# Optimization experiments

Hardware: AMD Instinct MI355X
Metric: run time of the kernel (lower is better)

The kernel has to match this reference:

```python
import jax, jax.numpy as jnp
import numpy as np

B, N, D = 16, 2048, 4        # batch, input points, input feature dim (x,y,e1,e2)
G = 45                        # folding grid side -> M = G*G = 2025 output points
M = G * G
CW = 512                      # codeword dim
H1, H2 = 64, 128              # encoder hidden dims
FH = 512                      # folding MLP hidden dim


def _glorot(key, shape):
    fan_in, fan_out = shape[0], shape[1]
    s = jnp.sqrt(2.0 / (fan_in + fan_out)).astype(jnp.float32)
    return jax.random.normal(key, shape, dtype=jnp.float32) * s


def setup_inputs() -> dict:
    key = jax.random.key(0)
    ks = jax.random.split(key, 16)
    inp = {
        "points": jax.random.normal(ks[0], (B, N, D), dtype=jnp.float32),
        # encoder shared MLP: D -> H1 -> H2 -> CW, max-pool over N
        "ew1": _glorot(ks[1], (D, H1)),  "eb1": jnp.zeros((H1,), jnp.float32),
        "ew2": _glorot(ks[2], (H1, H2)), "eb2": jnp.zeros((H2,), jnp.float32),
        "ew3": _glorot(ks[3], (H2, CW)), "eb3": jnp.zeros((CW,), jnp.float32),
        # folding decoder
        "f1w1": _glorot(ks[4], (CW + 2, FH)), "f1b1": jnp.zeros((FH,), jnp.float32),
        "f1w2": _glorot(ks[5], (FH, FH)),     "f1b2": jnp.zeros((FH,), jnp.float32),
        "f1w3": _glorot(ks[6], (FH, 3)),      "f1b3": jnp.zeros((3,), jnp.float32),
        "f2w1": _glorot(ks[7], (CW + 3, FH)), "f2b1": jnp.zeros((FH,), jnp.float32),
        "f2w2": _glorot(ks[8], (FH, FH)),     "f2b2": jnp.zeros((FH,), jnp.float32),
        "f2w3": _glorot(ks[9], (FH, 3)),      "f2b3": jnp.zeros((3,), jnp.float32),
    }
    # fixed 2D folding grid in [-0.3, 0.3]^2, (M, 2)
    lin = jnp.linspace(-0.3, 0.3, G, dtype=jnp.float32)
    gx, gy = jnp.meshgrid(lin, lin, indexing="ij")
    inp["grid"] = jnp.stack([gx.ravel(), gy.ravel()], axis=-1)
    return inp


def _encode(points, ew1, eb1, ew2, eb2, ew3, eb3):
    h = jax.nn.relu(points @ ew1 + eb1)     # (B, N, H1)
    h = jax.nn.relu(h @ ew2 + eb2)          # (B, N, H2)
    h = h @ ew3 + eb3                       # (B, N, CW)
    return jnp.max(h, axis=1)               # (B, CW) codeword theta


def _decode(theta, grid, f1w1, f1b1, f1w2, f1b2, f1w3, f1b3,
            f2w1, f2b1, f2w2, f2b2, f2w3, f2b3):
    th = jnp.broadcast_to(theta[:, None, :], (theta.shape[0], M, CW))
    g = jnp.broadcast_to(grid[None], (theta.shape[0], M, 2))
    # folding 1: (codeword, 2D grid) -> 3D
    x = jnp.concatenate([th, g], axis=-1)
    x = jax.nn.relu(x @ f1w1 + f1b1)
    x = jax.nn.relu(x @ f1w2 + f1b2)
    fold1 = x @ f1w3 + f1b3                 # (B, M, 3)
    # folding 2: (codeword, intermediate 3D) -> 3D
    x = jnp.concatenate([th, fold1], axis=-1)
    x = jax.nn.relu(x @ f2w1 + f2b1)
    x = jax.nn.relu(x @ f2w2 + f2b2)
    return x @ f2w3 + f2b3                  # (B, M, 3)


def _chamfer(a, b):
    # a: (B, N, 3), b: (B, M, 3); squared-distance chamfer, both directions
    a2 = jnp.sum(a * a, axis=-1)                          # (B, N)
    b2 = jnp.sum(b * b, axis=-1)                          # (B, M)
    ab = jnp.einsum("bnd,bmd->bnm", a, b)                  # (B, N, M)
    d2 = a2[:, :, None] + b2[:, None, :] - 2.0 * ab
    d2 = jnp.maximum(d2, 0.0)
    return jnp.mean(jnp.min(d2, axis=2)) + jnp.mean(jnp.min(d2, axis=1))


def reference(points, ew1, eb1, ew2, eb2, ew3, eb3, grid,
              f1w1, f1b1, f1w2, f1b2, f1w3, f1b3,
              f2w1, f2b1, f2w2, f2b2, f2w3, f2b3):
    theta = _encode(points, ew1, eb1, ew2, eb2, ew3, eb3)
    pc_out = _decode(theta, grid, f1w1, f1b1, f1w2, f1b2, f1w3, f1b3,
                     f2w1, f2b1, f2w2, f2b2, f2w3, f2b3)
    # pc_input: (x, y, sum of energy channels)  -> (B, N, 3)
    energy = jnp.sum(points[:, :, 2:], axis=-1, keepdims=True)
    pc_input = jnp.concatenate([points[:, :, :2], energy], axis=-1)
    loss = _chamfer(pc_input, pc_out)
    return theta, pc_out, loss
```

## Files before the change

### kernel.cpp

```cpp
#include <hip/hip_runtime.h>

#define NBATCH 16
#define NPTS   2048
#define MQ     2025
#define CWDIM  512
#define NROWS  32400

typedef __attribute__((ext_vector_type(8))) short bf16x8;
typedef __attribute__((ext_vector_type(4))) float f32x4;

__device__ __forceinline__ unsigned fkey(float f) {
  unsigned u = __float_as_uint(f);
  return (u & 0x80000000u) ? ~u : (u | 0x80000000u);
}
__device__ __forceinline__ float funkey(unsigned u) {
  unsigned v = (u & 0x80000000u) ? (u ^ 0x80000000u) : ~u;
  return __uint_as_float(v);
}
__device__ __forceinline__ unsigned short f2bf(float f) {
  unsigned u = __float_as_uint(f);
  u = (u + 0x7FFFu + ((u >> 16) & 1u)) >> 16;
  return (unsigned short)u;
}

__global__ __launch_bounds__(256) void prep_kernel(
    const float* __restrict__ ew2, const float* __restrict__ ew3,
    const float* __restrict__ f1w2, const float* __restrict__ f2w2,
    unsigned short* __restrict__ ew2T, unsigned short* __restrict__ ew3C,
    unsigned short* __restrict__ w2C, unsigned* __restrict__ zws)
{
  __shared__ float tile[32][33];
  const int blk = blockIdx.x;
  const int t = threadIdx.x;

  if (blk < 8) {
    const int kt = blk >> 2, nt = blk & 3;
    const int tx = t & 31, ty = t >> 5;
    #pragma unroll
    for (int j = 0; j < 4; ++j)
      tile[ty + 8 * j][tx] = ew2[(size_t)(kt * 32 + ty + 8 * j) * 128 + nt * 32 + tx];
    __syncthreads();
    #pragma unroll
    for (int j = 0; j < 4; ++j)
      ew2T[(size_t)(nt * 32 + ty + 8 * j) * 64 + kt * 32 + tx] = f2bf(tile[tx][ty + 8 * j]);
  } else if (blk < 40) {
    const int gid = (blk - 8) * 256 + t;
    const int c16 = gid & 15, hi = (gid >> 4) & 3, cblk = (gid >> 6) & 31, kblk = gid >> 11;
    const int col = cblk * 16 + c16;
    unsigned short tmp[8];
    #pragma unroll
    for (int j = 0; j < 8; ++j)
      tmp[j] = f2bf(ew3[(size_t)(kblk * 32 + hi * 8 + j) * 512 + col]);
    int4 pk;
    pk.x = (int)((unsigned)tmp[0] | ((unsigned)tmp[1] << 16));
    pk.y = (int)((unsigned)tmp[2] | ((unsigned)tmp[3] << 16));
    pk.z = (int)((unsigned)tmp[4] | ((unsigned)tmp[5] << 16));
    pk.w = (int)((unsigned)tmp[6] | ((unsigned)tmp[7] << 16));
    *(int4*)&ew3C[(size_t)gid * 8] = pk;
  } else if (blk < 296) {
    const int gid = (blk - 40) * 256 + t;
    const int s = gid >> 15;
    const int rem = gid & 32767;
    const int c16 = rem & 15, hi = (rem >> 4) & 3, cblk = (rem >> 6) & 31, kt = rem >> 11;
    const int col = cblk * 16 + c16;
    const float* src = s ? f2w2 : f1w2;
    unsigned short tmp[8];
    #pragma unroll
    for (int j = 0; j < 8; ++j)
      tmp[j] = f2bf(src[(size_t)(kt * 32 + hi * 8 + j) * 512 + col]);
    int4 pk;
    pk.x = (int)((unsigned)tmp[0] | ((unsigned)tmp[1] << 16));
    pk.y = (int)((unsigned)tmp[2] | ((unsigned)tmp[3] << 16));
    pk.z = (int)((unsigned)tmp[4] | ((unsigned)tmp[5] << 16));
    pk.w = (int)((unsigned)tmp[6] | ((unsigned)tmp[7] << 16));
    *(int4*)&w2C[(size_t)s * 262144 + (size_t)rem * 8] = pk;
  } else {
    const int idx = (blk - 296) * 256 + t;
    for (int i = idx; i < 24640; i += 6144) zws[i] = 0u;
  }
}

__global__ __launch_bounds__(512, 2) void enc2_kernel(
    const float* __restrict__ pts,
    const float* __restrict__ ew1, const float* __restrict__ eb1,
    const unsigned short* __restrict__ ew2T, const float* __restrict__ eb2,
    const unsigned short* __restrict__ ew3C, const float* __restrict__ eb3,
    unsigned* __restrict__ keys)
{
  __shared__ unsigned short h1s[64 * 64];
  __shared__ unsigned short h2s[64 * 128];
  __shared__ float s_pts[64][4];
  const int t = threadIdx.x;
  const int b = blockIdx.x >> 5, p0 = (blockIdx.x & 31) << 6;
  if (t < 64)
    *(float4*)&s_pts[t][0] = *(const float4*)(pts + ((size_t)b * NPTS + p0 + t) * 4);
  __syncthreads();

  {
    const int c = t & 63;
    const float w0 = ew1[c], w1 = ew1[64 + c], w2 = ew1[128 + c], w3 = ew1[192 + c];
    const float bb = eb1[c];
    #pragma unroll
    for (int i = 0; i < 8; ++i) {
      const int p = i * 8 + (t >> 6);
      float acc = bb + s_pts[p][0] * w0 + s_pts[p][1] * w1 + s_pts[p][2] * w2 + s_pts[p][3] * w3;
      unsigned byte = ((unsigned)p << 7) + ((unsigned)c << 1);
      byte ^= ((unsigned)(p & 7)) << 4;
      h1s[byte >> 1] = f2bf(fmaxf(acc, 0.f));
    }
  }
  __syncthreads();

  const int wv = t >> 6, lane = t & 63, l15 = lane & 15, hi = lane >> 4;

  {
    f32x4 acc[4];
    #pragma unroll
    for (int m = 0; m < 4; ++m) acc[m] = (f32x4){0.f, 0.f, 0.f, 0.f};
    const int col = 16 * wv + l15;
    #pragma unroll
    for (int kk = 0; kk < 64; kk += 32) {
      bf16x8 bv = *(const bf16x8*)(ew2T + (size_t)col * 64 + kk + hi * 8);
      #pragma unroll
      for (int m = 0; m < 4; ++m) {
        const int row = 16 * m + l15;
        unsigned byte = ((unsigned)row << 7) + ((unsigned)((kk + hi * 8)) << 1);
        byte ^= ((unsigned)(row & 7)) << 4;
        bf16x8 av = *(const bf16x8*)&h1s[byte >> 1];
        acc[m] = __builtin_amdgcn_mfma_f32_16x16x32_bf16(av, bv, acc[m], 0, 0, 0);
      }
    }
    const float b2c = eb2[col];
    #pragma unroll
    for (int m = 0; m < 4; ++m)
      #pragma unroll
      for (int r = 0; r < 4; ++r) {
        const int row = 16 * m + hi * 4 + r;
        unsigned byte = ((unsigned)row << 8) + ((unsigned)col << 1);
        byte ^= ((unsigned)(row & 7)) << 4;
        h2s[byte >> 1] = f2bf(fmaxf(acc[m][r] + b2c, 0.f));
      }
  }
  __syncthreads();

  {
    f32x4 acc[4][4];
    #pragma unroll
    for (int m = 0; m < 4; ++m)
      #pragma unroll
      for (int n = 0; n < 4; ++n) acc[m][n] = (f32x4){0.f, 0.f, 0.f, 0.f};
    #pragma unroll
    for (int kk = 0; kk < 128; kk += 32) {
      bf16x8 av[4];
      #pragma unroll
      for (int m = 0; m < 4; ++m) {
        const int row = 16 * m + l15;
        unsigned byte = ((unsigned)row << 8) + ((unsigned)(kk + hi * 8) << 1);
        byte ^= ((unsigned)(row & 7)) << 4;
        av[m] = *(const bf16x8*)&h2s[byte >> 1];
      }
      #pragma unroll
      for (int n = 0; n < 4; ++n) {
        bf16x8 bv = *(const bf16x8*)(ew3C +
            (size_t)(((kk >> 5) * 32 + 4 * wv + n) * 512) + lane * 8);
        #pragma unroll
        for (int m = 0; m < 4; ++m)
          acc[m][n] = __builtin_amdgcn_mfma_f32_16x16x32_bf16(av[m], bv, acc[m][n], 0, 0, 0);
      }
    }
    #pragma unroll
    for (int n = 0; n < 4; ++n) {
      const int col = 64 * wv + 16 * n + l15;
      float mx = -1e30f;
      #pragma unroll
      for (int m = 0; m < 4; ++m)
        #pragma unroll
        for (int r = 0; r < 4; ++r) mx = fmaxf(mx, acc[m][n][r]);
      mx = fmaxf(mx, __shfl_xor(mx, 16));
      mx = fmaxf(mx, __shfl_xor(mx, 32));
      if (hi == 0) atomicMax(&keys[b * CWDIM + col], fkey(mx + eb3[col]));
    }
  }
}

__global__ __launch_bounds__(256) void h1base_kernel(
    const unsigned* __restrict__ keys, float* __restrict__ theta_out,
    const float* __restrict__ f1w1, const float* __restrict__ f1b1,
    const float* __restrict__ f2w1, const float* __restrict__ f2b1,
    float* __restrict__ h1b)
{
  __shared__ float thl[256];
  const int t = threadIdx.x;
  const int gid = blockIdx.x * 256 + t;
  const int half = gid >> 14;
  const int rem = gid & 16383;
  const int stage = rem >> 13, bb = (rem >> 9) & 15, c = rem & 511;
  thl[t] = funkey(keys[bb * 512 + half * 256 + t]);
  if (gid < 8192) theta_out[gid] = funkey(keys[gid]);
  __syncthreads();
  const float* w = stage ? f2w1 : f1w1;
  float acc = (half == 0) ? (stage ? f2b1[c] : f1b1[c]) : 0.f;
  const float* wp = w + (size_t)(half * 256) * 512 + c;
  #pragma unroll 8
  for (int k = 0; k < 256; ++k) acc += thl[k] * wp[(size_t)k * 512];
  atomicAdd(&h1b[rem], acc);
}

struct Fold5Smem {
  unsigned short sA[64 * 512];
  float red[8][32][3];
  float ext[64][4];
  int   rowbb[64];
};

template <int ST>
__device__ __forceinline__ void fold5_stage(Fold5Smem& S, int t, int r0,
    const float* __restrict__ h1bg,
    const float* __restrict__ w1,
    const unsigned short* __restrict__ wst,
    const float* __restrict__ b2, const float* __restrict__ w3,
    const float* __restrict__ b3, float* __restrict__ out_pc)
{
  constexpr int NE = ST ? 3 : 2;
  const int wv = t >> 6, lane = t & 63, l15 = lane & 15, hi = lane >> 4;
  const int wm = wv >> 2, wn = wv & 3;

  __syncthreads();

  {
    const int row = t & 63;
    const int bb = S.rowbb[row];
    const float e0 = S.ext[row][0], e1 = S.ext[row][1];
    float e2 = 0.f;
    if (NE == 3) e2 = S.ext[row][2];
    const float* hb  = h1bg + ST * 8192 + bb * 512;
    const float* wr0 = w1 + (size_t)512 * 512;
    const float* wr1 = wr0 + 512;
    const float* wr2 = wr1 + 512;
    #pragma unroll
    for (int i = 0; i < 8; ++i) {
      const int ko = (t >> 6) * 8 + i;
      const int c0 = ko * 8;
      float v[8];
      #pragma unroll
      for (int hf = 0; hf < 2; ++hf) {
        float4 h = *(const float4*)(hb + c0 + hf * 4);
        float4 a = *(const float4*)(wr0 + c0 + hf * 4);
        float4 bq = *(const float4*)(wr1 + c0 + hf * 4);
        v[hf * 4 + 0] = h.x + e0 * a.x + e1 * bq.x;
        v[hf * 4 + 1] = h.y + e0 * a.y + e1 * bq.y;
        v[hf * 4 + 2] = h.z + e0 * a.z + e1 * bq.z;
        v[hf * 4 + 3] = h.w + e0 * a.w + e1 * bq.w;
        if (NE == 3) {
          float4 cq = *(const float4*)(wr2 + c0 + hf * 4);
          v[hf * 4 + 0] += e2 * cq.x; v[hf * 4 + 1] += e2 * cq.y;
          v[hf * 4 + 2] += e2 * cq.z; v[hf * 4 + 3] += e2 * cq.w;
        }
      }
      int4 pk;
      pk.x = (int)((unsigned)f2bf(fmaxf(v[0], 0.f)) | ((unsigned)f2bf(fmaxf(v[1], 0.f)) << 16));
      pk.y = (int)((unsigned)f2bf(fmaxf(v[2], 0.f)) | ((unsigned)f2bf(fmaxf(v[3], 0.f)) << 16));
      pk.z = (int)((unsigned)f2bf(fmaxf(v[4], 0.f)) | ((unsigned)f2bf(fmaxf(v[5], 0.f)) << 16));
      pk.w = (int)((unsigned)f2bf(fmaxf(v[6], 0.f)) | ((unsigned)f2bf(fmaxf(v[7], 0.f)) << 16));
      *(int4*)&S.sA[(unsigned)(((ko >> 2) * 4 + (row >> 4)) * 512 + (ko & 3) * 128 + (row & 15) * 8)] = pk;
    }
  }
  __syncthreads();

  float p[2][4][3];
  #pragma unroll
  for (int m = 0; m < 2; ++m)
    #pragma unroll
    for (int r = 0; r < 4; ++r)
      #pragma unroll
      for (int jj = 0; jj < 3; ++jj) p[m][r][jj] = 0.f;

  #pragma unroll 1
  for (int pass = 0; pass < 2; ++pass) {
    f32x4 acc[2][4];
    #pragma unroll
    for (int m = 0; m < 2; ++m)
      #pragma unroll
      for (int n = 0; n < 4; ++n) acc[m][n] = (f32x4){0.f, 0.f, 0.f, 0.f};

    const unsigned short* wb = wst + (size_t)(pass * 16 + wn * 4) * 512 + lane * 8;

    #pragma unroll 2
    for (int kt = 0; kt < 16; ++kt) {
      bf16x8 bv[4];
      #pragma unroll
      for (int n = 0; n < 4; ++n)
        bv[n] = *(const bf16x8*)(wb + (size_t)(kt * 32 + n) * 512);
      const unsigned abase = (unsigned)(kt * 4 + 2 * wm) * 512 + (unsigned)lane * 8;
      bf16x8 a0 = *(const bf16x8*)&S.sA[abase];
      bf16x8 a1 = *(const bf16x8*)&S.sA[abase + 512];
      __builtin_amdgcn_s_setprio(1);
      #pragma unroll
      for (int n = 0; n < 4; ++n) {
        acc[0][n] = __builtin_amdgcn_mfma_f32_16x16x32_bf16(a0, bv[n], acc[0][n], 0, 0, 0);
        acc[1][n] = __builtin_amdgcn_mfma_f32_16x16x32_bf16(a1, bv[n], acc[1][n], 0, 0, 0);
      }
      __builtin_amdgcn_s_setprio(0);
    }

    #pragma unroll
    for (int n = 0; n < 4; ++n) {
      const int colG = pass * 256 + wn * 64 + 16 * n + l15;
      const float b2c = b2[colG];
      const float w30 = w3[colG * 3 + 0], w31 = w3[colG * 3 + 1], w32 = w3[colG * 3 + 2];
      #pragma unroll
      for (int m = 0; m < 2; ++m)
        #pragma unroll
        for (int r = 0; r < 4; ++r) {
          const float h = fmaxf(acc[m][n][r] + b2c, 0.f);
          p[m][r][0] += h * w30; p[m][r][1] += h * w31; p[m][r][2] += h * w32;
        }
    }
  }

  #pragma unroll
  for (int m = 0; m < 2; ++m)
    #pragma unroll
    for (int r = 0; r < 4; ++r)
      #pragma unroll
      for (int jj = 0; jj < 3; ++jj) {
        float v = p[m][r][jj];
        v += __shfl_xor(v, 1); v += __shfl_xor(v, 2);
        v += __shfl_xor(v, 4); v += __shfl_xor(v, 8);
        p[m][r][jj] = v;
      }
  if (l15 == 0) {
    #pragma unroll
    for (int m = 0; m < 2; ++m)
      #pragma unroll
      for (int r = 0; r < 4; ++r) {
        const int rl = 16 * m + hi * 4 + r;
        S.red[wv][rl][0] = p[m][r][0];
        S.red[wv][rl][1] = p[m][r][1];
        S.red[wv][rl][2] = p[m][r][2];
      }
  }
  __syncthreads();

  if (t < 192) {
    const int row = t / 3, jj = t - (t / 3) * 3;
    const int wg = (row >> 5) * 4, rl = row & 31;
    float v = b3[jj] + S.red[wg][rl][jj] + S.red[wg + 1][rl][jj]
                     + S.red[wg + 2][rl][jj] + S.red[wg + 3][rl][jj];
    if (ST == 0) S.ext[row][jj] = v;
    else if (r0 + row < NROWS) out_pc[(size_t)(r0 + row) * 3 + jj] = v;
  }
  __syncthreads();
}

__global__ __launch_bounds__(512, 2) void fold5_kernel(
    const float* __restrict__ grid2, const float* __restrict__ h1b,
    const unsigned short* __restrict__ w2C,
    const float* __restrict__ f1w1, const float* __restrict__ f1b2,
    const float* __restrict__ f1w3, const float* __restrict__ f1b3,
    const float* __restrict__ f2w1, const float* __restrict__ f2b2,
    const float* __restrict__ f2w3, const float* __restrict__ f2b3,
    float* __restrict__ out_pc)
{
  __shared__ Fold5Smem S;
  const int t = threadIdx.x;
  const int r0 = blockIdx.x * 64;

  if (t < 64) {
    const int r = r0 + t;
    const int bb = min(r / MQ, NBATCH - 1);
    S.rowbb[t] = bb;
    const int m = min(r - bb * MQ, MQ - 1);
    S.ext[t][0] = grid2[m * 2 + 0];
    S.ext[t][1] = grid2[m * 2 + 1];
    S.ext[t][2] = 0.f;
    S.ext[t][3] = 0.f;
  }

  fold5_stage<0>(S, t, r0, h1b, f1w1, w2C,          f1b2, f1w3, f1b3, nullptr);
  fold5_stage<1>(S, t, r0, h1b, f2w1, w2C + 262144, f2b2, f2w3, f2b3, out_pc);
}

__global__ __launch_bounds__(256) void cham_kernel(
    const float* __restrict__ pts, const float* __restrict__ pc,
    float* __restrict__ lacc, float* __restrict__ loss)
{
  __shared__ float s0[2048], s1[2048], s2[2048];
  const int t = threadIdx.x;
  const int side = blockIdx.x >> 9;
  const int ib = blockIdx.x & 511;
  const int b = ib >> 5;

  if (side == 0) {
    const int n0 = (ib & 31) << 6;
    const float* pcb = pc + (size_t)b * (MQ * 3);
    for (int i = t; i < MQ * 3; i += 256) {
      float v = pcb[i];
      int m = i / 3, j = i - m * 3;
      if (j == 0) s0[m] = v; else if (j == 1) s1[m] = v; else s2[m] = v;
    }
    for (int i = MQ + t; i < 2048; i += 256) { s0[i] = 1e30f; s1[i] = 1e30f; s2[i] = 1e30f; }
    __syncthreads();

    const int pid = t >> 4, q = t & 15;
    float ax[4], ay[4], az[4], mn[4];
    #pragma unroll
    for (int j = 0; j < 4; ++j) {
      const int n = n0 + pid * 4 + j;
      float4 P = *(const float4*)(pts + ((size_t)b * NPTS + n) * 4);
      ax[j] = P.x; ay[j] = P.y; az[j] = P.z + P.w; mn[j] = 1e30f;
    }
    #pragma unroll 4
    for (int i = 0; i < 32; ++i) {
      const int m4 = q * 4 + i * 64;
      float4 bx = *(const float4*)&s0[m4];
      float4 by = *(const float4*)&s1[m4];
      float4 bz = *(const float4*)&s2[m4];
      #pragma unroll
      for (int j = 0; j < 4; ++j) {
        float d0, dx, dy, dz;
        dx = ax[j] - bx.x; dy = ay[j] - by.x; dz = az[j] - bz.x; d0 = dx*dx + dy*dy + dz*dz; mn[j] = fminf(mn[j], d0);
        dx = ax[j] - bx.y; dy = ay[j] - by.y; dz = az[j] - bz.y; d0 = dx*dx + dy*dy + dz*dz; mn[j] = fminf(mn[j], d0);
        dx = ax[j] - bx.z; dy = ay[j] - by.z; dz = az[j] - bz.z; d0 = dx*dx + dy*dy + dz*dz; mn[j] = fminf(mn[j], d0);
        dx = ax[j] - bx.w; dy = ay[j] - by.w; dz = az[j] - bz.w; d0 = dx*dx + dy*dy + dz*dz; mn[j] = fminf(mn[j], d0);
      }
    }
    #pragma unroll
    for (int j = 0; j < 4; ++j) {
      mn[j] = fminf(mn[j], __shfl_xor(mn[j], 1));
      mn[j] = fminf(mn[j], __shfl_xor(mn[j], 2));
      mn[j] = fminf(mn[j], __shfl_xor(mn[j], 4));
      mn[j] = fminf(mn[j], __shfl_xor(mn[j], 8));
    }
    float v = (q == 0) ? (mn[0] + mn[1] + mn[2] + mn[3]) : 0.f;
    v += __shfl_xor(v, 16); v += __shfl_xor(v, 32);
    if ((t & 63) == 0) atomicAdd(lacc, v);
  } else {
    const int m0 = (ib & 31) << 6;
    for (int i = t; i < NPTS; i += 256) {
      float4 pp = *(const float4*)(pts + ((size_t)b * NPTS + i) * 4);
      s0[i] = pp.x; s1[i] = pp.y; s2[i] = pp.z + pp.w;
    }
    __syncthreads();

    const int pid = t >> 4, q = t & 15;
    float bx[4], by[4], bz[4], mn[4];
    bool vld[4];
    #pragma unroll
    for (int j = 0; j < 4; ++j) {
      const int m = m0 + pid * 4 + j;
      vld[j] = (m < MQ);
      const int mc = vld[j] ? m : (MQ - 1);
      bx[j] = pc[(size_t)b * (MQ * 3) + mc * 3 + 0];
      by[j] = pc[(size_t)b * (MQ * 3) + mc * 3 + 1];
      bz[j] = pc[(size_t)b * (MQ * 3) + mc * 3 + 2];
      mn[j] = 1e30f;
    }
    #pragma unroll 4
    for (int i = 0; i < 32; ++i) {
      const int n4 = q * 4 + i * 64;
      float4 axv = *(const float4*)&s0[n4];
      float4 ayv = *(const float4*)&s1[n4];
      float4 azv = *(const float4*)&s2[n4];
      #pragma unroll
      for (int j = 0; j < 4; ++j) {
        float d0, dx, dy, dz;
        dx = axv.x - bx[j]; dy = ayv.x - by[j]; dz = azv.x - bz[j]; d0 = dx*dx + dy*dy + dz*dz; mn[j] = fminf(mn[j], d0);
        dx = axv.y - bx[j]; dy = ayv.y - by[j]; dz = azv.y - bz[j]; d0 = dx*dx + dy*dy + dz*dz; mn[j] = fminf(mn[j], d0);
        dx = axv.z - bx[j]; dy = ayv.z - by[j]; dz = azv.z - bz[j]; d0 = dx*dx + dy*dy + dz*dz; mn[j] = fminf(mn[j], d0);
        dx = axv.w - bx[j]; dy = ayv.w - by[j]; dz = azv.w - bz[j]; d0 = dx*dx + dy*dy + dz*dz; mn[j] = fminf(mn[j], d0);
      }
    }
    #pragma unroll
    for (int j = 0; j < 4; ++j) {
      mn[j] = fminf(mn[j], __shfl_xor(mn[j], 1));
      mn[j] = fminf(mn[j], __shfl_xor(mn[j], 2));
      mn[j] = fminf(mn[j], __shfl_xor(mn[j], 4));
      mn[j] = fminf(mn[j], __shfl_xor(mn[j], 8));
    }
    float v = 0.f;
    if (q == 0) {
      #pragma unroll
      for (int j = 0; j < 4; ++j) if (vld[j]) v += mn[j];
    }
    v += __shfl_xor(v, 16); v += __shfl_xor(v, 32);
    if ((t & 63) == 0) atomicAdd(lacc + 1, v);
  }

  __syncthreads();
  if (t == 0) {
    __threadfence();
    unsigned old = atomicAdd((unsigned*)(lacc + 2), 1u);
    if (old == 1023u) {
      float l0 = atomicAdd(lacc, 0.f);
      float l1 = atomicAdd(lacc + 1, 0.f);
      loss[0] = l0 * (1.0f / (NBATCH * NPTS)) + l1 * (1.0f / (NBATCH * MQ));
    }
  }
}

extern "C" void kernel_launch(void* const* d_in, const int* in_sizes, int n_in,
                              void* d_out, int out_size, void* d_ws, size_t ws_size,
                              hipStream_t stream) {
  const float* pts  = (const float*)d_in[0];
  const float* ew1  = (const float*)d_in[1];
  const float* eb1  = (const float*)d_in[2];
  const float* ew2  = (const float*)d_in[3];
  const float* eb2  = (const float*)d_in[4];
  const float* ew3  = (const float*)d_in[5];
  const float* eb3  = (const float*)d_in[6];
  const float* f1w1 = (const float*)d_in[7];
  const float* f1b1 = (const float*)d_in[8];
  const float* f1w2 = (const float*)d_in[9];
  const float* f1b2 = (const float*)d_in[10];
  const float* f1w3 = (const float*)d_in[11];
  const float* f1b3 = (const float*)d_in[12];
  const float* f2w1 = (const float*)d_in[13];
  const float* f2b1 = (const float*)d_in[14];
  const float* f2w2 = (const float*)d_in[15];
  const float* f2b2 = (const float*)d_in[16];
  const float* f2w3 = (const float*)d_in[17];
  const float* f2b3 = (const float*)d_in[18];
  const float* grid2= (const float*)d_in[19];

  float* out = (float*)d_out;
  unsigned* keys       = (unsigned*)d_ws;
  float* lacc          = (float*)((char*)d_ws + 32768);
  float* h1b           = (float*)((char*)d_ws + 33024);
  unsigned short* w2C  = (unsigned short*)((char*)d_ws + 98560);
  unsigned short* ew2T = (unsigned short*)((char*)d_ws + 1147136);
  unsigned short* ew3C = (unsigned short*)((char*)d_ws + 1163520);

  prep_kernel<<<320, 256, 0, stream>>>(ew2, ew3, f1w2, f2w2,
                                       ew2T, ew3C, w2C, (unsigned*)d_ws);
  enc2_kernel<<<512, 512, 0, stream>>>(pts, ew1, eb1, ew2T, eb2, ew3C, eb3, keys);
  h1base_kernel<<<128, 256, 0, stream>>>(keys, out, f1w1, f1b1, f2w1, f2b1, h1b);
  fold5_kernel<<<507, 512, 0, stream>>>(grid2, h1b, w2C,
                                        f1w1, f1b2, f1w3, f1b3,
                                        f2w1, f2b2, f2w3, f2b3,
                                        out + 8192);
  cham_kernel<<<1024, 256, 0, stream>>>(pts, out + 8192, lacc,
                                        out + 8192 + 97200);
}
```

Before: 253.4 us.

## Widen fold MFMA tiles per wave and use expanded-norm chamfer distances

The fold kernel now has each of the 8 waves compute all 64 rows against its own 64 output columns in a single pass. This replaces the 2x4 wave split that needed two passes, so each wave loads each weight tile once and reuses it across four A tiles. The cost is 64 accumulator registers per wave, which forces launch bounds down to one block per SIMD pair and lowers occupancy. The chamfer kernel precomputes squared norms into shared memory and evaluates distances as three FMAs plus a norm, applying the other point's norm and the clamp only after the min. Padding values change from 1e30 to 100 so the norm stays finite.

```diff
diff --git a/kernel.cpp b/kernel.cpp
--- a/kernel.cpp
+++ b/kernel.cpp
@@ -206,15 +206,15 @@
   atomicAdd(&h1b[rem], acc);
 }
 
-struct Fold5Smem {
+struct Fold6Smem {
   unsigned short sA[64 * 512];
-  float red[8][32][3];
+  float red[8][64][3];
   float ext[64][4];
   int   rowbb[64];
 };
 
 template <int ST>
-__device__ __forceinline__ void fold5_stage(Fold5Smem& S, int t, int r0,
+__device__ __forceinline__ void fold6_stage(Fold6Smem& S, int t, int r0,
     const float* __restrict__ h1bg,
     const float* __restrict__ w1,
     const unsigned short* __restrict__ wst,
@@ -223,7 +223,6 @@
 {
   constexpr int NE = ST ? 3 : 2;
   const int wv = t >> 6, lane = t & 63, l15 = lane & 15, hi = lane >> 4;
-  const int wm = wv >> 2, wn = wv & 3;
 
   __syncthreads();
 
@@ -267,59 +266,57 @@
   }
   __syncthreads();
 
-  float p[2][4][3];
+  f32x4 acc[4][4];
   #pragma unroll
-  for (int m = 0; m < 2; ++m)
+  for (int m = 0; m < 4; ++m)
+    #pragma unroll
+    for (int n = 0; n < 4; ++n) acc[m][n] = (f32x4){0.f, 0.f, 0.f, 0.f};
+
+  const unsigned short* wb = wst + (size_t)(4 * wv) * 512 + lane * 8;
+
+  #pragma unroll 2
+  for (int kt = 0; kt < 16; ++kt) {
+    bf16x8 bv[4];
+    #pragma unroll
+    for (int n = 0; n < 4; ++n)
+      bv[n] = *(const bf16x8*)(wb + (size_t)(kt * 32 + n) * 512);
+    bf16x8 a[4];
+    #pragma unroll
+    for (int m = 0; m < 4; ++m)
+      a[m] = *(const bf16x8*)&S.sA[(unsigned)(kt * 4 + m) * 512 + (unsigned)lane * 8];
+    __builtin_amdgcn_s_setprio(1);
+    #pragma unroll
+    for (int n = 0; n < 4; ++n)
+      #pragma unroll
+      for (int m = 0; m < 4; ++m)
+        acc[m][n] = __builtin_amdgcn_mfma_f32_16x16x32_bf16(a[m], bv[n], acc[m][n], 0, 0, 0);
+    __builtin_amdgcn_s_setprio(0);
+  }
+
+  float p[4][4][3];
+  #pragma unroll
+  for (int m = 0; m < 4; ++m)
     #pragma unroll
     for (int r = 0; r < 4; ++r)
       #pragma unroll
       for (int jj = 0; jj < 3; ++jj) p[m][r][jj] = 0.f;
 
-  #pragma unroll 1
-  for (int pass = 0; pass < 2; ++pass) {
-    f32x4 acc[2][4];
-    #pragma unroll
-    for (int m = 0; m < 2; ++m)
-      #pragma unroll
-      for (int n = 0; n < 4; ++n) acc[m][n] = (f32x4){0.f, 0.f, 0.f, 0.f};
-
-    const unsigned short* wb = wst + (size_t)(pass * 16 + wn * 4) * 512 + lane * 8;
-
-    #pragma unroll 2
-    for (int kt = 0; kt < 16; ++kt) {
-      bf16x8 bv[4];
-      #pragma unroll
-      for (int n = 0; n < 4; ++n)
-        bv[n] = *(const bf16x8*)(wb + (size_t)(kt * 32 + n) * 512);
-      const unsigned abase = (unsigned)(kt * 4 + 2 * wm) * 512 + (unsigned)lane * 8;
-      bf16x8 a0 = *(const bf16x8*)&S.sA[abase];
-      bf16x8 a1 = *(const bf16x8*)&S.sA[abase + 512];
-      __builtin_amdgcn_s_setprio(1);
-      #pragma unroll
-      for (int n = 0; n < 4; ++n) {
-        acc[0][n] = __builtin_amdgcn_mfma_f32_16x16x32_bf16(a0, bv[n], acc[0][n], 0, 0, 0);
-        acc[1][n] = __builtin_amdgcn_mfma_f32_16x16x32_bf16(a1, bv[n], acc[1][n], 0, 0, 0);
-      }
-      __builtin_amdgcn_s_setprio(0);
-    }
-
-    #pragma unroll
-    for (int n = 0; n < 4; ++n) {
-      const int colG = pass * 256 + wn * 64 + 16 * n + l15;
-      const float b2c = b2[colG];
-      const float w30 = w3[colG * 3 + 0], w31 = w3[colG * 3 + 1], w32 = w3[colG * 3 + 2];
-      #pragma unroll
-      for (int m = 0; m < 2; ++m)
-        #pragma unroll
-        for (int r = 0; r < 4; ++r) {
-          const float h = fmaxf(acc[m][n][r] + b2c, 0.f);
-          p[m][r][0] += h * w30; p[m][r][1] += h * w31; p[m][r][2] += h * w32;
-        }
-    }
-  }
-
   #pragma unroll
-  for (int m = 0; m < 2; ++m)
+  for (int n = 0; n < 4; ++n) {
+    const int colG = 64 * wv + 16 * n + l15;
+    const float b2c = b2[colG];
+    const float w30 = w3[colG * 3 + 0], w31 = w3[colG * 3 + 1], w32 = w3[colG * 3 + 2];
+    #pragma unroll
+    for (int m = 0; m < 4; ++m)
+      #pragma unroll
+      for (int r = 0; r < 4; ++r) {
+        const float h = fmaxf(acc[m][n][r] + b2c, 0.f);
+        p[m][r][0] += h * w30; p[m][r][1] += h * w31; p[m][r][2] += h * w32;
+      }
+  }
+
+  #pragma unroll
+  for (int m = 0; m < 4; ++m)
     #pragma unroll
     for (int r = 0; r < 4; ++r)
       #pragma unroll
@@ -331,29 +328,29 @@
       }
   if (l15 == 0) {
     #pragma unroll
-    for (int m = 0; m < 2; ++m)
+    for (int m = 0; m < 4; ++m)
       #pragma unroll
       for (int r = 0; r < 4; ++r) {
-        const int rl = 16 * m + hi * 4 + r;
-        S.red[wv][rl][0] = p[m][r][0];
-        S.red[wv][rl][1] = p[m][r][1];
-        S.red[wv][rl][2] = p[m][r][2];
+        const int row = 16 * m + hi * 4 + r;
+        S.red[wv][row][0] = p[m][r][0];
+        S.red[wv][row][1] = p[m][r][1];
+        S.red[wv][row][2] = p[m][r][2];
       }
   }
   __syncthreads();
 
   if (t < 192) {
     const int row = t / 3, jj = t - (t / 3) * 3;
-    const int wg = (row >> 5) * 4, rl = row & 31;
-    float v = b3[jj] + S.red[wg][rl][jj] + S.red[wg + 1][rl][jj]
-                     + S.red[wg + 2][rl][jj] + S.red[wg + 3][rl][jj];
+    float v = b3[jj];
+    #pragma unroll
+    for (int w = 0; w < 8; ++w) v += S.red[w][row][jj];
     if (ST == 0) S.ext[row][jj] = v;
     else if (r0 + row < NROWS) out_pc[(size_t)(r0 + row) * 3 + jj] = v;
   }
   __syncthreads();
 }
 
-__global__ __launch_bounds__(512, 2) void fold5_kernel(
+__global__ __launch_bounds__(512, 1) void fold6_kernel(
     const float* __restrict__ grid2, const float* __restrict__ h1b,
     const unsigned short* __restrict__ w2C,
     const float* __restrict__ f1w1, const float* __restrict__ f1b2,
@@ -362,7 +359,7 @@
     const float* __restrict__ f2w3, const float* __restrict__ f2b3,
     float* __restrict__ out_pc)
 {
-  __shared__ Fold5Smem S;
+  __shared__ Fold6Smem S;
   const int t = threadIdx.x;
   const int r0 = blockIdx.x * 64;
 
@@ -377,15 +374,15 @@
     S.ext[t][3] = 0.f;
   }
 
-  fold5_stage<0>(S, t, r0, h1b, f1w1, w2C,          f1b2, f1w3, f1b3, nullptr);
-  fold5_stage<1>(S, t, r0, h1b, f2w1, w2C + 262144, f2b2, f2w3, f2b3, out_pc);
+  fold6_stage<0>(S, t, r0, h1b, f1w1, w2C,          f1b2, f1w3, f1b3, nullptr);
+  fold6_stage<1>(S, t, r0, h1b, f2w1, w2C + 262144, f2b2, f2w3, f2b3, out_pc);
 }
 
 __global__ __launch_bounds__(256) void cham_kernel(
     const float* __restrict__ pts, const float* __restrict__ pc,
     float* __restrict__ lacc, float* __restrict__ loss)
 {
-  __shared__ float s0[2048], s1[2048], s2[2048];
+  __shared__ float s0[2048], s1[2048], s2[2048], s3[2048];
   const int t = threadIdx.x;
   const int side = blockIdx.x >> 9;
   const int ib = blockIdx.x & 511;
@@ -399,16 +396,22 @@
       int m = i / 3, j = i - m * 3;
       if (j == 0) s0[m] = v; else if (j == 1) s1[m] = v; else s2[m] = v;
     }
-    for (int i = MQ + t; i < 2048; i += 256) { s0[i] = 1e30f; s1[i] = 1e30f; s2[i] = 1e30f; }
+    for (int i = MQ + t; i < 2048; i += 256) { s0[i] = 100.f; s1[i] = 100.f; s2[i] = 100.f; }
     __syncthreads();
+    for (int i = t; i < 2048; i += 256)
+      s3[i] = s0[i] * s0[i] + s1[i] * s1[i] + s2[i] * s2[i];
+    __syncthreads();
 
     const int pid = t >> 4, q = t & 15;
-    float ax[4], ay[4], az[4], mn[4];
+    float nx[4], ny[4], nz[4], a2[4], mn[4];
     #pragma unroll
     for (int j = 0; j < 4; ++j) {
       const int n = n0 + pid * 4 + j;
       float4 P = *(const float4*)(pts + ((size_t)b * NPTS + n) * 4);
-      ax[j] = P.x; ay[j] = P.y; az[j] = P.z + P.w; mn[j] = 1e30f;
+      const float az = P.z + P.w;
+      nx[j] = -2.f * P.x; ny[j] = -2.f * P.y; nz[j] = -2.f * az;
+      a2[j] = P.x * P.x + P.y * P.y + az * az;
+      mn[j] = 1e30f;
     }
     #pragma unroll 4
     for (int i = 0; i < 32; ++i) {
@@ -416,13 +419,14 @@
       float4 bx = *(const float4*)&s0[m4];
       float4 by = *(const float4*)&s1[m4];
       float4 bz = *(const float4*)&s2[m4];
+      float4 bq = *(const float4*)&s3[m4];
       #pragma unroll
       for (int j = 0; j < 4; ++j) {
-        float d0, dx, dy, dz;
-        dx = ax[j] - bx.x; dy = ay[j] - by.x; dz = az[j] - bz.x; d0 = dx*dx + dy*dy + dz*dz; mn[j] = fminf(mn[j], d0);
-        dx = ax[j] - bx.y; dy = ay[j] - by.y; dz = az[j] - bz.y; d0 = dx*dx + dy*dy + dz*dz; mn[j] = fminf(mn[j], d0);
-        dx = ax[j] - bx.z; dy = ay[j] - by.z; dz = az[j] - bz.z; d0 = dx*dx + dy*dy + dz*dz; mn[j] = fminf(mn[j], d0);
-        dx = ax[j] - bx.w; dy = ay[j] - by.w; dz = az[j] - bz.w; d0 = dx*dx + dy*dy + dz*dz; mn[j] = fminf(mn[j], d0);
+        float d0 = fmaf(nx[j], bx.x, fmaf(ny[j], by.x, fmaf(nz[j], bz.x, bq.x)));
+        float d1 = fmaf(nx[j], bx.y, fmaf(ny[j], by.y, fmaf(nz[j], bz.y, bq.y)));
+        float d2 = fmaf(nx[j], bx.z, fmaf(ny[j], by.z, fmaf(nz[j], bz.z, bq.z)));
+        float d3 = fmaf(nx[j], bx.w, fmaf(ny[j], by.w, fmaf(nz[j], bz.w, bq.w)));
+        mn[j] = fminf(mn[j], fminf(fminf(d0, d1), fminf(d2, d3)));
       }
     }
     #pragma unroll
@@ -432,43 +436,52 @@
       mn[j] = fminf(mn[j], __shfl_xor(mn[j], 4));
       mn[j] = fminf(mn[j], __shfl_xor(mn[j], 8));
     }
-    float v = (q == 0) ? (mn[0] + mn[1] + mn[2] + mn[3]) : 0.f;
+    float v = 0.f;
+    if (q == 0) {
+      #pragma unroll
+      for (int j = 0; j < 4; ++j) v += fmaxf(mn[j] + a2[j], 0.f);
+    }
     v += __shfl_xor(v, 16); v += __shfl_xor(v, 32);
     if ((t & 63) == 0) atomicAdd(lacc, v);
   } else {
     const int m0 = (ib & 31) << 6;
     for (int i = t; i < NPTS; i += 256) {
       float4 pp = *(const float4*)(pts + ((size_t)b * NPTS + i) * 4);
-      s0[i] = pp.x; s1[i] = pp.y; s2[i] = pp.z + pp.w;
+      const float az = pp.z + pp.w;
+      s0[i] = pp.x; s1[i] = pp.y; s2[i] = az;
+      s3[i] = pp.x * pp.x + pp.y * pp.y + az * az;
     }
     __syncthreads();
 
     const int pid = t >> 4, q = t & 15;
-    float bx[4], by[4], bz[4], mn[4];
+    float nx[4], ny[4], nz[4], b2r[4], mn[4];
     bool vld[4];
     #pragma unroll
     for (int j = 0; j < 4; ++j) {
       const int m = m0 + pid * 4 + j;
       vld[j] = (m < MQ);
       const int mc = vld[j] ? m : (MQ - 1);
-      bx[j] = pc[(size_t)b * (MQ * 3) + mc * 3 + 0];
-      by[j] = pc[(size_t)b * (MQ * 3) + mc * 3 + 1];
-      bz[j] = pc[(size_t)b * (MQ * 3) + mc * 3 + 2];
+      const float bx = pc[(size_t)b * (MQ * 3) + mc * 3 + 0];
+      const float by = pc[(size_t)b * (MQ * 3) + mc * 3 + 1];
+      const float bz = pc[(size_t)b * (MQ * 3) + mc * 3 + 2];
+      nx[j] = -2.f * bx; ny[j] = -2.f * by; nz[j] = -2.f * bz;
+      b2r[j] = bx * bx + by * by + bz * bz;
       mn[j] = 1e30f;
     }
     #pragma unroll 4
     for (int i = 0; i < 32; ++i) {
       const int n4 = q * 4 + i * 64;
-      float4 axv = *(const float4*)&s0[n4];
-      float4 ayv = *(const float4*)&s1[n4];
-      float4 azv = *(const float4*)&s2[n4];
+      float4 ax = *(const float4*)&s0[n4];
+      float4 ay = *(const float4*)&s1[n4];
+      float4 az = *(const float4*)&s2[n4];
+      float4 aq = *(const float4*)&s3[n4];
       #pragma unroll
       for (int j = 0; j < 4; ++j) {
-        float d0, dx, dy, dz;
-        dx = axv.x - bx[j]; dy = ayv.x - by[j]; dz = azv.x - bz[j]; d0 = dx*dx + dy*dy + dz*dz; mn[j] = fminf(mn[j], d0);
-        dx = axv.y - bx[j]; dy = ayv.y - by[j]; dz = azv.y - bz[j]; d0 = dx*dx + dy*dy + dz*dz; mn[j] = fminf(mn[j], d0);
-        dx = axv.z - bx[j]; dy = ayv.z - by[j]; dz = azv.z - bz[j]; d0 = dx*dx + dy*dy + dz*dz; mn[j] = fminf(mn[j], d0);
-        dx = axv.w - bx[j]; dy = ayv.w - by[j]; dz = azv.w - bz[j]; d0 = dx*dx + dy*dy + dz*dz; mn[j] = fminf(mn[j], d0);
+        float d0 = fmaf(nx[j], ax.x, fmaf(ny[j], ay.x, fmaf(nz[j], az.x, aq.x)));
+        float d1 = fmaf(nx[j], ax.y, fmaf(ny[j], ay.y, fmaf(nz[j], az.y, aq.y)));
+        float d2 = fmaf(nx[j], ax.z, fmaf(ny[j], ay.z, fmaf(nz[j], az.z, aq.z)));
+        float d3 = fmaf(nx[j], ax.w, fmaf(ny[j], ay.w, fmaf(nz[j], az.w, aq.w)));
+        mn[j] = fminf(mn[j], fminf(fminf(d0, d1), fminf(d2, d3)));
       }
     }
     #pragma unroll
@@ -481,7 +494,7 @@
     float v = 0.f;
     if (q == 0) {
       #pragma unroll
-      for (int j = 0; j < 4; ++j) if (vld[j]) v += mn[j];
+      for (int j = 0; j < 4; ++j) if (vld[j]) v += fmaxf(mn[j] + b2r[j], 0.f);
     }
     v += __shfl_xor(v, 16); v += __shfl_xor(v, 32);
     if ((t & 63) == 0) atomicAdd(lacc + 1, v);
@@ -535,7 +548,7 @@
                                        ew2T, ew3C, w2C, (unsigned*)d_ws);
   enc2_kernel<<<512, 512, 0, stream>>>(pts, ew1, eb1, ew2T, eb2, ew3C, eb3, keys);
   h1base_kernel<<<128, 256, 0, stream>>>(keys, out, f1w1, f1b1, f2w1, f2b1, h1b);
-  fold5_kernel<<<507, 512, 0, stream>>>(grid2, h1b, w2C,
+  fold6_kernel<<<507, 512, 0, stream>>>(grid2, h1b, w2C,
                                         f1w1, f1b2, f1w3, f1b3,
                                         f2w1, f2b2, f2w3, f2b3,
                                         out + 8192);
```

Measured after the change: 263.7 us. 4.0% more time.
